# Optimization experiments

Measured on AMD Instinct MI355X. Metric: run time of the kernel, lower is better.

The kernel has to match this reference:

```python
import jax, jax.numpy as jnp
import numpy as np

B, L, V, E, H2, M, OOV = 128, 400, 50000, 512, 1024, 1024, 50


def setup_inputs() -> dict:
    key = jax.random.key(0)
    ks = jax.random.split(key, 14)
    s = 0.02
    return {
        "y": jax.random.randint(ks[0], (B,), 0, V),
        "h": jax.random.normal(ks[1], (1, B, H2), jnp.float32),
        "memory_bank": jax.random.normal(ks[2], (B, L, M), jnp.float32),
        "src_mask": jnp.ones((B, L), jnp.float32),
        "max_num_oovs": OOV,
        "src_oov": jax.random.randint(ks[3], (B, L), 0, V + OOV),
        # learned parameters (PyTorch Linear y = x @ W + b with W stored [in, out])
        "emb": jax.random.normal(ks[4], (V, E), jnp.float32) * s,
        "W_ih": jax.random.normal(ks[5], (E, 3 * H2), jnp.float32) * s,   # GRU input weights (r|z|n)
        "W_hh": jax.random.normal(ks[6], (H2, 3 * H2), jnp.float32) * s,  # GRU hidden weights (r|z|n)
        "b_ih": jnp.zeros((3 * H2,), jnp.float32),
        "b_hh": jnp.zeros((3 * H2,), jnp.float32),
        "W_mem": jax.random.normal(ks[7], (M, H2), jnp.float32) * s,      # attention memory_project (no bias)
        "W_dec": jax.random.normal(ks[8], (H2, H2), jnp.float32) * s,     # attention decode_project
        "b_dec": jnp.zeros((H2,), jnp.float32),
        "v": jax.random.normal(ks[9], (H2,), jnp.float32) * s,            # attention score vector (no bias)
        "W_pgen": jax.random.normal(ks[10], (M + H2 + E, 1), jnp.float32) * s,
        "b_pgen": jnp.zeros((1,), jnp.float32),
        "W_v1": jax.random.normal(ks[11], (M + H2, H2), jnp.float32) * s,
        "b_v1": jnp.zeros((H2,), jnp.float32),
        "W_v2": jax.random.normal(ks[12], (H2, V), jnp.float32) * s,
        "b_v2": jnp.zeros((V,), jnp.float32),
    }


def reference(y, h, memory_bank, src_mask, max_num_oovs, src_oov,
              emb, W_ih, W_hh, b_ih, b_hh, W_mem, W_dec, b_dec, v,
              W_pgen, b_pgen, W_v1, b_v1, W_v2, b_v2):
    # --- embedding lookup (single decode step) ---
    y_emb = emb[y]                                    # [B, E]
    h0 = h[-1]                                        # [B, H2]

    # --- one-step GRU (PyTorch gate order r, z, n); dropout is identity (eval) ---
    gi = y_emb @ W_ih + b_ih                          # [B, 3*H2]
    gh = h0 @ W_hh + b_hh
    i_r, i_z, i_n = jnp.split(gi, 3, axis=-1)
    h_r, h_z, h_n = jnp.split(gh, 3, axis=-1)
    r = jax.nn.sigmoid(i_r + h_r)
    z = jax.nn.sigmoid(i_z + h_z)
    n = jnp.tanh(i_n + r * h_n)
    h_next = (1.0 - z) * n + z * h0                   # [B, H2]

    # --- concat (Bahdanau) attention with masked softmax ---
    enc_feat = jnp.einsum('blm,mh->blh', memory_bank, W_mem)   # [B, L, H2]
    dec_feat = h_next @ W_dec + b_dec                           # [B, H2]
    scores = jnp.tanh(enc_feat + dec_feat[:, None, :]) @ v     # [B, L]
    attn = jax.nn.softmax(scores, axis=1) * src_mask
    attn_dist = attn / attn.sum(axis=1, keepdims=True)         # renormalized masked softmax
    context = jnp.einsum('bl,blm->bm', attn_dist, memory_bank) # [B, M]

    # --- vocab distribution ---
    vd_in = jnp.concatenate([context, h_next], axis=1)          # [B, M+H2]
    logits = (vd_in @ W_v1 + b_v1) @ W_v2 + b_v2                # [B, V]
    vocab_dist = jax.nn.softmax(logits, axis=1)

    # --- generation gate ---
    pg_in = jnp.concatenate([context, h_next, y_emb], axis=1)   # [B, M+H2+E]
    p_gen = jax.nn.sigmoid(pg_in @ W_pgen + b_pgen)             # [B, 1]

    # --- copy mechanism: scatter attention mass into extended vocab ---
    vocab_dist_ = p_gen * vocab_dist
    attn_dist_ = (1.0 - p_gen) * attn_dist
    bsz = vocab_dist_.shape[0]
    if max_num_oovs > 0:
        vocab_dist_ = jnp.concatenate(
            [vocab_dist_, jnp.zeros((bsz, max_num_oovs), vocab_dist_.dtype)], axis=1)
    rows = jnp.arange(bsz)[:, None]
    final_dist = vocab_dist_.at[rows, src_oov].add(attn_dist_)  # [B, V+OOV]

    return final_dist, h_next[None], context, attn_dist, p_gen
```

## Files before the change

### kernel.cpp

```cpp
#include <hip/hip_runtime.h>

#define B_   128
#define L_   400
#define V_   50000
#define E_   512
#define H2_  1024
#define M_   1024
#define OOV_ 50
#define VE_  50050
#define BL_  51200

typedef __attribute__((ext_vector_type(8))) short short8;
typedef __attribute__((ext_vector_type(4))) float f32x4;

__device__ __forceinline__ unsigned short f2bf(float f){
  unsigned int u = __builtin_bit_cast(unsigned int, f);
  u = (u + 0x7FFFu + ((u >> 16) & 1u)) >> 16;
  return (unsigned short)u;
}
__device__ __forceinline__ float bf2f(unsigned short s){
  unsigned int u = ((unsigned int)s) << 16;
  return __builtin_bit_cast(float, u);
}

__device__ __forceinline__ void gl_lds16(const void* g, void* l){
  __builtin_amdgcn_global_load_lds(
      (const __attribute__((address_space(1))) unsigned int*)g,
      (__attribute__((address_space(3))) unsigned int*)l, 16, 0, 0);
}

__device__ __forceinline__ float wredsum(float v){
  #pragma unroll
  for (int o = 32; o > 0; o >>= 1) v += __shfl_xor(v, o);
  return v;
}
__device__ __forceinline__ float wredmax(float v){
  #pragma unroll
  for (int o = 32; o > 0; o >>= 1) v = fmaxf(v, __shfl_xor(v, o));
  return v;
}

__global__ void embed_gather_kernel(const int* __restrict__ y, const float* __restrict__ emb,
                                    float* __restrict__ yemb){
  int idx = blockIdx.x * 256 + threadIdx.x;
  int b  = idx >> 7;
  int c4 = (idx & 127) << 2;
  float4 v = *(const float4*)(emb + (size_t)y[b] * E_ + c4);
  *(float4*)(yemb + (size_t)b * E_ + c4) = v;
}

__global__ void mb_convert_kernel(const float* __restrict__ mb, unsigned char* __restrict__ mbT){
  int u = blockIdx.x * 256 + threadIdx.x;
  int gr  = u >> 7;
  int m16 = u & 127;
  const float* src = mb + (size_t)gr * 1024 + m16 * 8;
  float4 f0 = *(const float4*)src;
  float4 f1 = *(const float4*)(src + 4);
  uint4 w;
  w.x = (unsigned)f2bf(f0.x) | ((unsigned)f2bf(f0.y) << 16);
  w.y = (unsigned)f2bf(f0.z) | ((unsigned)f2bf(f0.w) << 16);
  w.z = (unsigned)f2bf(f1.x) | ((unsigned)f2bf(f1.y) << 16);
  w.w = (unsigned)f2bf(f1.z) | ((unsigned)f2bf(f1.w) << 16);
  int panel = gr >> 7, r = gr & 127;
  int ks = m16 >> 3, c16 = m16 & 7;
  size_t dst = (size_t)panel * 262144 + (size_t)ks * 16384
             + (size_t)((r * 128 + c16 * 16) ^ ((r & 7) << 4));
  *(uint4*)(mbT + dst) = w;
}

__global__ void wmem_transposeT_kernel(const float* __restrict__ W, unsigned char* __restrict__ WTt){
  __shared__ float tile[32][33];
  int n0 = blockIdx.x * 32, k0 = blockIdx.y * 32;
  int tx = threadIdx.x, ty = threadIdx.y;
  #pragma unroll
  for (int i = 0; i < 32; i += 8) tile[ty + i][tx] = W[(size_t)(k0 + ty + i) * H2_ + n0 + tx];
  __syncthreads();
  int id = ty * 32 + tx;
  if (id < 128){
    int nn = id & 31, k16 = id >> 5;
    int col = n0 + nn, kb = k0 + k16 * 8;
    uint4 w;
    w.x = (unsigned)f2bf(tile[k16*8+0][nn]) | ((unsigned)f2bf(tile[k16*8+1][nn]) << 16);
    w.y = (unsigned)f2bf(tile[k16*8+2][nn]) | ((unsigned)f2bf(tile[k16*8+3][nn]) << 16);
    w.z = (unsigned)f2bf(tile[k16*8+4][nn]) | ((unsigned)f2bf(tile[k16*8+5][nn]) << 16);
    w.w = (unsigned)f2bf(tile[k16*8+6][nn]) | ((unsigned)f2bf(tile[k16*8+7][nn]) << 16);
    int cpn = col >> 7, r = col & 127;
    int ks = kb >> 6, c16 = (kb & 63) >> 3;
    size_t dst = (size_t)cpn * 262144 + (size_t)ks * 16384
               + (size_t)((r * 128 + c16 * 16) ^ ((r & 7) << 4));
    *(uint4*)(WTt + dst) = w;
  }
}

__launch_bounds__(256)
__global__ void gemm128_kernel(const float* __restrict__ A, int lda,
                               const float* __restrict__ W, int ldw,
                               const float* __restrict__ bias,
                               float* __restrict__ C, int ldc,
                               int N, int kChunk, int addBias)
{
  int tid = threadIdx.x;
  int wv = tid >> 6, lane = tid & 63, lr = lane & 15, lhi = lane >> 4;
  int colBase = blockIdx.x * 128 + wv * 32;
  int colL[2];
  colL[0] = min(colBase + lr, N - 1);
  colL[1] = min(colBase + 16 + lr, N - 1);
  int k0 = blockIdx.y * kChunk;

  f32x4 zero = {0.f, 0.f, 0.f, 0.f};
  f32x4 acc[8][2];
  #pragma unroll
  for (int r = 0; r < 8; r++){ acc[r][0] = zero; acc[r][1] = zero; }

  int nks = kChunk >> 5;
  for (int ks = 0; ks < nks; ++ks){
    int k = k0 + ks * 32 + lhi * 8;
    short8 bf[2];
    #pragma unroll
    for (int cf = 0; cf < 2; cf++){
      #pragma unroll
      for (int j = 0; j < 8; j++)
        bf[cf][j] = (short)f2bf(W[(size_t)(k + j) * ldw + colL[cf]]);
    }
    #pragma unroll
    for (int rf = 0; rf < 8; rf++){
      const float* ap = A + (size_t)(rf * 16 + lr) * lda + k;
      float4 a0 = *(const float4*)ap;
      float4 a1 = *(const float4*)(ap + 4);
      short8 af;
      af[0]=(short)f2bf(a0.x); af[1]=(short)f2bf(a0.y); af[2]=(short)f2bf(a0.z); af[3]=(short)f2bf(a0.w);
      af[4]=(short)f2bf(a1.x); af[5]=(short)f2bf(a1.y); af[6]=(short)f2bf(a1.z); af[7]=(short)f2bf(a1.w);
      acc[rf][0] = __builtin_amdgcn_mfma_f32_16x16x32_bf16(af, bf[0], acc[rf][0], 0, 0, 0);
      acc[rf][1] = __builtin_amdgcn_mfma_f32_16x16x32_bf16(af, bf[1], acc[rf][1], 0, 0, 0);
    }
  }

  bool addB = addBias && (blockIdx.y == 0);
  #pragma unroll
  for (int cf = 0; cf < 2; cf++){
    int col = colBase + cf * 16 + lr;
    bool ok = col < N;
    float bv = addB ? bias[colL[cf]] : 0.f;
    #pragma unroll
    for (int rf = 0; rf < 8; rf++)
      #pragma unroll
      for (int i = 0; i < 4; i++){
        int row = rf * 16 + lhi * 4 + i;
        if (ok) atomicAdd(&C[(size_t)row * ldc + col], acc[rf][cf][i] + bv);
      }
  }
}

__launch_bounds__(256)
__global__ void gemm_v1_kernel(const float* __restrict__ A1, const float* __restrict__ A2,
                               const float* __restrict__ W,
                               const float* __restrict__ bias,
                               float* __restrict__ C, int N, int kChunk)
{
  int tid = threadIdx.x;
  int wv = tid >> 6, lane = tid & 63, lr = lane & 15, lhi = lane >> 4;
  int colBase = blockIdx.x * 128 + wv * 32;
  int halfY = gridDim.y >> 1;
  const float* Asrc = (blockIdx.y < halfY) ? A1 : A2;
  int yk = (blockIdx.y < halfY) ? blockIdx.y : (blockIdx.y - halfY);
  int k0 = yk * kChunk;
  int wk0 = blockIdx.y * kChunk;

  f32x4 zero = {0.f, 0.f, 0.f, 0.f};
  f32x4 acc[8][2];
  #pragma unroll
  for (int r = 0; r < 8; r++){ acc[r][0] = zero; acc[r][1] = zero; }

  int nks = kChunk >> 5;
  for (int ks = 0; ks < nks; ++ks){
    int k  = k0 + ks * 32 + lhi * 8;
    int wk = wk0 + ks * 32 + lhi * 8;
    short8 bf[2];
    #pragma unroll
    for (int cf = 0; cf < 2; cf++){
      #pragma unroll
      for (int j = 0; j < 8; j++)
        bf[cf][j] = (short)f2bf(W[(size_t)(wk + j) * H2_ + colBase + cf * 16 + lr]);
    }
    #pragma unroll
    for (int rf = 0; rf < 8; rf++){
      const float* ap = Asrc + (size_t)(rf * 16 + lr) * 1024 + k;
      float4 a0 = *(const float4*)ap;
      float4 a1 = *(const float4*)(ap + 4);
      short8 af;
      af[0]=(short)f2bf(a0.x); af[1]=(short)f2bf(a0.y); af[2]=(short)f2bf(a0.z); af[3]=(short)f2bf(a0.w);
      af[4]=(short)f2bf(a1.x); af[5]=(short)f2bf(a1.y); af[6]=(short)f2bf(a1.z); af[7]=(short)f2bf(a1.w);
      acc[rf][0] = __builtin_amdgcn_mfma_f32_16x16x32_bf16(af, bf[0], acc[rf][0], 0, 0, 0);
      acc[rf][1] = __builtin_amdgcn_mfma_f32_16x16x32_bf16(af, bf[1], acc[rf][1], 0, 0, 0);
    }
  }

  bool addB = (blockIdx.y == 0);
  #pragma unroll
  for (int cf = 0; cf < 2; cf++){
    int col = colBase + cf * 16 + lr;
    float bv = addB ? bias[col] : 0.f;
    #pragma unroll
    for (int rf = 0; rf < 8; rf++)
      #pragma unroll
      for (int i = 0; i < 4; i++){
        int row = rf * 16 + lhi * 4 + i;
        atomicAdd(&C[(size_t)row * H2_ + col], acc[rf][cf][i] + bv);
      }
  }
}

__launch_bounds__(256)
__global__ void gemm_bfA_kernel(const unsigned short* __restrict__ A,
                                const float* __restrict__ W,
                                const float* __restrict__ bias,
                                float* __restrict__ C0, float* __restrict__ C1,
                                int N, int kChunk)
{
  int tid = threadIdx.x;
  int wv = tid >> 6, lane = tid & 63, lr = lane & 15, lhi = lane >> 4;
  int colBase = blockIdx.x * 128 + wv * 32;
  int colL[2];
  colL[0] = min(colBase + lr, N - 1);
  colL[1] = min(colBase + 16 + lr, N - 1);
  int k0 = blockIdx.y * kChunk;
  float* Cw = (blockIdx.y == 0) ? C0 : C1;

  f32x4 zero = {0.f, 0.f, 0.f, 0.f};
  f32x4 acc[8][2];
  #pragma unroll
  for (int r = 0; r < 8; r++){ acc[r][0] = zero; acc[r][1] = zero; }

  int nks = kChunk >> 5;
  for (int ks = 0; ks < nks; ++ks){
    int k = k0 + ks * 32 + lhi * 8;
    short8 bf[2];
    #pragma unroll
    for (int cf = 0; cf < 2; cf++){
      #pragma unroll
      for (int j = 0; j < 8; j++)
        bf[cf][j] = (short)f2bf(W[(size_t)(k + j) * N + colL[cf]]);
    }
    #pragma unroll
    for (int rf = 0; rf < 8; rf++){
      short8 af = *(const short8*)(A + (size_t)(rf * 16 + lr) * 1024 + k);
      acc[rf][0] = __builtin_amdgcn_mfma_f32_16x16x32_bf16(af, bf[0], acc[rf][0], 0, 0, 0);
      acc[rf][1] = __builtin_amdgcn_mfma_f32_16x16x32_bf16(af, bf[1], acc[rf][1], 0, 0, 0);
    }
  }

  bool addB = (blockIdx.y == 0);
  #pragma unroll
  for (int cf = 0; cf < 2; cf++){
    int col = colBase + cf * 16 + lr;
    bool ok = col < N;
    float bv = addB ? bias[colL[cf]] : 0.f;
    #pragma unroll
    for (int rf = 0; rf < 8; rf++)
      #pragma unroll
      for (int i = 0; i < 4; i++){
        int row = rf * 16 + lhi * 4 + i;
        if (ok) Cw[(size_t)row * V_ + col] = acc[rf][cf][i] + bv;
      }
  }
}

__global__ void gru_gates_kernel(const float* __restrict__ gi, const float* __restrict__ gh,
                                 const float* __restrict__ bih, const float* __restrict__ bhh,
                                 const float* __restrict__ h0, float* __restrict__ hn){
  int idx = blockIdx.x * 256 + threadIdx.x;
  int b = idx >> 10, j = idx & 1023;
  const float* gib = gi + (size_t)b * 3072;
  const float* ghb = gh + (size_t)b * 3072;
  float ir = gib[j]        + bih[j],        hr = ghb[j]        + bhh[j];
  float iz = gib[j + 1024] + bih[j + 1024], hz = ghb[j + 1024] + bhh[j + 1024];
  float in_= gib[j + 2048] + bih[j + 2048], hnv= ghb[j + 2048] + bhh[j + 2048];
  float r = 1.f / (1.f + __expf(-(ir + hr)));
  float z = 1.f / (1.f + __expf(-(iz + hz)));
  float n = tanhf(in_ + r * hnv);
  hn[idx] = (1.f - z) * n + z * h0[idx];
}

__launch_bounds__(512, 3)
__global__ void scores_kernel(const unsigned char* __restrict__ mbT,
                              const unsigned char* __restrict__ WTt,
                              const float* __restrict__ dec, const float* __restrict__ vvec,
                              float* __restrict__ scr)
{
  __shared__ __align__(16) unsigned char LDSm[65536];
  const int tid = threadIdx.x, lane = tid & 63;
  const int wv = tid >> 6, lr = lane & 15, lhi = lane >> 4;
  const int wru = wv >> 2, wcu = wv & 3;

  int p = blockIdx.x;
  int lid = (p & 7) * 400 + (p >> 3);
  int rp = lid >> 3, cp = lid & 7;
  int r0 = rp << 7;

  int wvu = __builtin_amdgcn_readfirstlane(wv);
  const unsigned char* seg = (wvu < 4 ? mbT + (size_t)rp * 262144
                                      : WTt + (size_t)cp * 262144)
                             + (wvu & 3) * 4096 + lane * 16;
  const int segLds = (wvu & 3) * 4096 + (wvu < 4 ? 0 : 16384);

  int aoff[4], boff[2];
  #pragma unroll
  for (int rf = 0; rf < 4; rf++){
    int row = wru * 64 + rf * 16 + lr;
    aoff[rf] = (row * 128 + lhi * 16) ^ ((row & 7) << 4);
  }
  #pragma unroll
  for (int cf = 0; cf < 2; cf++){
    int col = wcu * 32 + cf * 16 + lr;
    boff[cf] = ((col * 128 + lhi * 16) ^ ((col & 7) << 4)) + 16384;
  }

  f32x4 zero = {0.f, 0.f, 0.f, 0.f};
  f32x4 acc[4][2];
  #pragma unroll
  for (int rf = 0; rf < 4; rf++){ acc[rf][0] = zero; acc[rf][1] = zero; }

  #pragma unroll
  for (int j = 0; j < 4; j++)
    gl_lds16(seg + j * 1024, &LDSm[segLds + j * 1024]);

  #pragma unroll 1
  for (int t = 0; t < 16; ++t){
    const int cur = (t & 1) << 15;
    if (t < 15){
      const unsigned char* s = seg + (size_t)(t + 1) * 16384;
      const int nb = ((t + 1) & 1) << 15;
      #pragma unroll
      for (int j = 0; j < 4; j++)
        gl_lds16(s + j * 1024, &LDSm[nb + segLds + j * 1024]);
      asm volatile("s_waitcnt vmcnt(4)" ::: "memory");
    } else {
      asm volatile("s_waitcnt vmcnt(0)" ::: "memory");
    }
    __builtin_amdgcn_sched_barrier(0);
    __builtin_amdgcn_s_barrier();
    __builtin_amdgcn_sched_barrier(0);
    #pragma unroll
    for (int k2 = 0; k2 < 2; k2++){
      short8 af[4], bfr[2];
      #pragma unroll
      for (int rf = 0; rf < 4; rf++) af[rf]  = *(const short8*)&LDSm[cur + (aoff[rf] ^ (k2 << 6))];
      #pragma unroll
      for (int cf = 0; cf < 2; cf++) bfr[cf] = *(const short8*)&LDSm[cur + (boff[cf] ^ (k2 << 6))];
      __builtin_amdgcn_s_setprio(1);
      #pragma unroll
      for (int rf = 0; rf < 4; rf++)
        #pragma unroll
        for (int cf = 0; cf < 2; cf++)
          acc[rf][cf] = __builtin_amdgcn_mfma_f32_16x16x32_bf16(af[rf], bfr[cf], acc[rf][cf], 0, 0, 0);
      __builtin_amdgcn_s_setprio(0);
    }
    __builtin_amdgcn_sched_barrier(0);
    asm volatile("s_waitcnt lgkmcnt(0)" ::: "memory");
    __builtin_amdgcn_s_barrier();
    __builtin_amdgcn_sched_barrier(0);
  }

  int colb = (cp << 7) + wcu * 32 + lr;
  float vv0 = vvec[colb], vv1 = vvec[colb + 16];
  #pragma unroll
  for (int rf = 0; rf < 4; rf++){
    #pragma unroll
    for (int i = 0; i < 4; i++){
      int grow = r0 + wru * 64 + rf * 16 + lhi * 4 + i;
      int bb = grow / 400;
      const float* dp = dec + (size_t)bb * 1024 + colb;
      float x0 = acc[rf][0][i] + dp[0];
      float x1 = acc[rf][1][i] + dp[16];
      float part = (1.f - 2.f / (__expf(2.f * x0) + 1.f)) * vv0
                 + (1.f - 2.f / (__expf(2.f * x1) + 1.f)) * vv1;
      part += __shfl_xor(part, 1);
      part += __shfl_xor(part, 2);
      part += __shfl_xor(part, 4);
      part += __shfl_xor(part, 8);
      if (lr == 0) atomicAdd(&scr[grow], part);
    }
  }
}

__global__ void attn_softmax_kernel(const float* __restrict__ scores, const float* __restrict__ mask,
                                    float* __restrict__ attn){
  int b = blockIdx.x, t = threadIdx.x;
  int wv = t >> 6, lane = t & 63;
  __shared__ float red[4];
  float s0 = (t < 400)       ? scores[b * 400 + t]       : -1e30f;
  float s1 = (t + 256 < 400) ? scores[b * 400 + t + 256] : -1e30f;
  float m = wredmax(fmaxf(s0, s1));
  if (lane == 0) red[wv] = m;
  __syncthreads();
  float M = fmaxf(fmaxf(red[0], red[1]), fmaxf(red[2], red[3]));
  __syncthreads();
  float e0 = (t < 400)       ? __expf(s0 - M) * mask[b * 400 + t]       : 0.f;
  float e1 = (t + 256 < 400) ? __expf(s1 - M) * mask[b * 400 + t + 256] : 0.f;
  float s = wredsum(e0 + e1);
  if (lane == 0) red[wv] = s;
  __syncthreads();
  float inv = 1.f / (red[0] + red[1] + red[2] + red[3]);
  if (t < 400)       attn[b * 400 + t]       = e0 * inv;
  if (t + 256 < 400) attn[b * 400 + t + 256] = e1 * inv;
}

__launch_bounds__(256)
__global__ void context_kernel(const float* __restrict__ attn, const unsigned char* __restrict__ mbT,
                               float* __restrict__ ctx){
  int b = blockIdx.y, lc = blockIdx.x, t = threadIdx.x;
  int u = t & 127;
  int half = t >> 7;
  __shared__ float a[100];
  if (t < 100) a[t] = attn[b * 400 + lc * 100 + t];
  __syncthreads();
  int ks = u >> 3, c16 = u & 7;
  float s[8];
  #pragma unroll
  for (int j = 0; j < 8; j++) s[j] = 0.f;
  for (int l = half; l < 100; l += 2){
    int gr = b * 400 + lc * 100 + l;
    int panel = gr >> 7, r = gr & 127;
    const unsigned char* pp = mbT + (size_t)panel * 262144 + (size_t)ks * 16384
                              + (size_t)((r * 128 + c16 * 16) ^ ((r & 7) << 4));
    short8 v = *(const short8*)pp;
    float al = a[l];
    #pragma unroll
    for (int j = 0; j < 8; j++) s[j] += al * bf2f((unsigned short)v[j]);
  }
  float* cp = ctx + (size_t)b * M_ + u * 8;
  #pragma unroll
  for (int j = 0; j < 8; j++) atomicAdd(cp + j, s[j]);
}

__global__ void pgen_kernel(const float* __restrict__ ctx, const float* __restrict__ hn,
                            const float* __restrict__ yemb,
                            const float* __restrict__ Wp, const float* __restrict__ bp,
                            float* __restrict__ pg){
  int b = blockIdx.x, t = threadIdx.x, wv = t >> 6, lane = t & 63;
  __shared__ float red[4];
  float s = 0.f;
  for (int i = t; i < 1024; i += 256) s += ctx[(size_t)b * 1024 + i] * Wp[i];
  for (int i = t; i < 1024; i += 256) s += hn[(size_t)b * 1024 + i] * Wp[1024 + i];
  for (int i = t; i < 512;  i += 256) s += yemb[(size_t)b * 512 + i] * Wp[2048 + i];
  s = wredsum(s);
  if (lane == 0) red[wv] = s;
  __syncthreads();
  if (t == 0){
    float S = red[0] + red[1] + red[2] + red[3] + bp[0];
    pg[b] = 1.f / (1.f + __expf(-S));
  }
}

__global__ void hid2bf_kernel(const float* __restrict__ hid, unsigned short* __restrict__ hb){
  int idx = blockIdx.x * 256 + threadIdx.x;
  float4 v = *(const float4*)(hid + (size_t)idx * 4);
  ushort2 p0 = {f2bf(v.x), f2bf(v.y)};
  ushort2 p1 = {f2bf(v.z), f2bf(v.w)};
  *(ushort2*)(hb + (size_t)idx * 4)     = p0;
  *(ushort2*)(hb + (size_t)idx * 4 + 2) = p1;
}

__global__ void vocab_softmax_kernel(float* __restrict__ lg0, const float* __restrict__ lg1,
                                     const float* __restrict__ pg,
                                     const float* __restrict__ attn, const int* __restrict__ soov,
                                     float* __restrict__ fin){
  int b = blockIdx.x, t = threadIdx.x, wv = t >> 6, lane = t & 63;
  __shared__ float redm[16], reds[16];
  float* l0 = lg0 + (size_t)b * V_;
  const float* l1 = lg1 + (size_t)b * V_;
  float m = -1e30f, s = 0.f;
  for (int i = t; i < V_; i += 1024){
    float l = l0[i] + l1[i];
    l0[i] = l;
    float mn = fmaxf(m, l);
    s = s * __expf(m - mn) + __expf(l - mn);
    m = mn;
  }
  #pragma unroll
  for (int o = 32; o > 0; o >>= 1){
    float mo = __shfl_xor(m, o), so = __shfl_xor(s, o);
    float mn = fmaxf(m, mo);
    s = s * __expf(m - mn) + so * __expf(mo - mn);
    m = mn;
  }
  if (lane == 0){ redm[wv] = m; reds[wv] = s; }
  __syncthreads();
  float M = -1e30f;
  #pragma unroll
  for (int w = 0; w < 16; w++) M = fmaxf(M, redm[w]);
  float S = 0.f;
  #pragma unroll
  for (int w = 0; w < 16; w++) S += reds[w] * __expf(redm[w] - M);
  float pgb = pg[b];
  float scale = pgb / S;
  float* fb = fin + (size_t)b * VE_;
  for (int i = t; i < V_; i += 1024) fb[i] = __expf(l0[i] - M) * scale;
  for (int i = V_ + t; i < VE_; i += 1024) fb[i] = 0.f;
  __syncthreads();
  float om = 1.f - pgb;
  if (t < 400) atomicAdd(&fb[soov[b * 400 + t]], om * attn[b * 400 + t]);
}

extern "C" void kernel_launch(void* const* d_in, const int* in_sizes, int n_in,
                              void* d_out, int out_size, void* d_ws, size_t ws_size,
                              hipStream_t stream)
{
  const int*   y     = (const int*)  d_in[0];
  const float* hin   = (const float*)d_in[1];
  const float* mb    = (const float*)d_in[2];
  const float* mask  = (const float*)d_in[3];
  const int*   soov  = (const int*)  d_in[5];
  const float* emb   = (const float*)d_in[6];
  const float* W_ih  = (const float*)d_in[7];
  const float* W_hh  = (const float*)d_in[8];
  const float* b_ih  = (const float*)d_in[9];
  const float* b_hh  = (const float*)d_in[10];
  const float* W_mem = (const float*)d_in[11];
  const float* W_dec = (const float*)d_in[12];
  const float* b_dec = (const float*)d_in[13];
  const float* vvec  = (const float*)d_in[14];
  const float* W_pg  = (const float*)d_in[15];
  const float* b_pg  = (const float*)d_in[16];
  const float* W_v1  = (const float*)d_in[17];
  const float* b_v1  = (const float*)d_in[18];
  const float* W_v2  = (const float*)d_in[19];
  const float* b_v2  = (const float*)d_in[20];

  float* out   = (float*)d_out;
  float* fin   = out;
  float* hnext = out + (size_t)B_ * VE_;
  float* ctx   = hnext + (size_t)B_ * H2_;
  float* attn  = ctx + (size_t)B_ * M_;
  float* pg    = attn + (size_t)B_ * L_;

  float* ws   = (float*)d_ws;
  float* yemb = ws;
  float* gi   = ws + 65536;
  float* gh   = gi + 393216;
  float* dec  = gh + 393216;
  float* scr  = dec + 131072;
  float* hid  = scr + 51200;
  float* lg0  = hid + 131072;
  unsigned short* hidbf = (unsigned short*)(lg0 + 6400000);
  unsigned char*  WTt   = (unsigned char*)(hidbf + 131072);
  unsigned char*  mbT   = WTt + 2097152;
  float* lg1  = (float*)mbT;

  hipMemsetAsync(gi, 0, (size_t)(393216 + 393216 + 131072 + 51200) * 4, stream);
  hipMemsetAsync(hid, 0, (size_t)131072 * 4, stream);
  hipMemsetAsync(ctx, 0, (size_t)B_ * M_ * 4, stream);

  embed_gather_kernel<<<64, 256, 0, stream>>>(y, emb, yemb);
  wmem_transposeT_kernel<<<dim3(32, 32), dim3(32, 8), 0, stream>>>(W_mem, WTt);
  mb_convert_kernel<<<25600, 256, 0, stream>>>(mb, mbT);

  gemm128_kernel<<<dim3(24, 2), 256, 0, stream>>>(yemb, E_,  W_ih, 3 * H2_, nullptr, gi, 3 * H2_, 3 * H2_, 256, 0);
  gemm128_kernel<<<dim3(24, 4), 256, 0, stream>>>(hin,  H2_, W_hh, 3 * H2_, nullptr, gh, 3 * H2_, 3 * H2_, 256, 0);
  gru_gates_kernel<<<512, 256, 0, stream>>>(gi, gh, b_ih, b_hh, hin, hnext);
  gemm128_kernel<<<dim3(8, 4), 256, 0, stream>>>(hnext, H2_, W_dec, H2_, b_dec, dec, H2_, H2_, 256, 1);

  scores_kernel<<<3200, 512, 0, stream>>>(mbT, WTt, dec, vvec, scr);
  attn_softmax_kernel<<<128, 256, 0, stream>>>(scr, mask, attn);
  context_kernel<<<dim3(4, 128), 256, 0, stream>>>(attn, mbT, ctx);

  pgen_kernel<<<128, 256, 0, stream>>>(ctx, hnext, yemb, W_pg, b_pg, pg);
  gemm_v1_kernel<<<dim3(8, 8), 256, 0, stream>>>(ctx, hnext, W_v1, b_v1, hid, H2_, 256);
  hid2bf_kernel<<<128, 256, 0, stream>>>(hid, hidbf);
  gemm_bfA_kernel<<<dim3(391, 2), 256, 0, stream>>>(hidbf, W_v2, b_v2, lg0, lg1, V_, 512);

  vocab_softmax_kernel<<<128, 1024, 0, stream>>>(lg0, lg1, pg, attn, soov, fin);
}
```

Baseline: 598.0 us.

## Fuse small launches and overlap memory-bank conversion with GRU GEMMs

Merges the memset, embedding gather, W_mem transpose and part of the memory-bank bf16 conversion into one pre-kernel. The rest of the conversion is split into chunks that ride along with the GRU GEMM, gate and decode-projection kernels, so the bandwidth-bound conversion overlaps the small, under-occupied GEMMs. The attention softmax is folded into the context kernel, and p_gen is folded into the W_v1 GEMM kernel, which now writes per-K-slice partials instead of using atomics. This cuts launch count and idle time, at the cost of heterogeneous blocks inside each kernel and more complex buffer aliasing.

```diff
diff --git a/kernel.cpp b/kernel.cpp
--- a/kernel.cpp
+++ b/kernel.cpp
@@ -40,17 +40,8 @@
   return v;
 }
 
-__global__ void embed_gather_kernel(const int* __restrict__ y, const float* __restrict__ emb,
-                                    float* __restrict__ yemb){
-  int idx = blockIdx.x * 256 + threadIdx.x;
-  int b  = idx >> 7;
-  int c4 = (idx & 127) << 2;
-  float4 v = *(const float4*)(emb + (size_t)y[b] * E_ + c4);
-  *(float4*)(yemb + (size_t)b * E_ + c4) = v;
-}
-
-__global__ void mb_convert_kernel(const float* __restrict__ mb, unsigned char* __restrict__ mbT){
-  int u = blockIdx.x * 256 + threadIdx.x;
+__device__ __forceinline__ void mb_convert_unit(const float* __restrict__ mb,
+                                                unsigned char* __restrict__ mbT, int u){
   int gr  = u >> 7;
   int m16 = u & 127;
   const float* src = mb + (size_t)gr * 1024 + m16 * 8;
@@ -68,32 +59,56 @@
   *(uint4*)(mbT + dst) = w;
 }
 
-__global__ void wmem_transposeT_kernel(const float* __restrict__ W, unsigned char* __restrict__ WTt){
+__global__ void pre_kernel(const float* __restrict__ mb, unsigned char* __restrict__ mbT,
+                           const float* __restrict__ Wm, unsigned char* __restrict__ WTt,
+                           const int* __restrict__ y, const float* __restrict__ emb,
+                           float* __restrict__ yemb, float* __restrict__ zeroA,
+                           float* __restrict__ ctx)
+{
   __shared__ float tile[32][33];
-  int n0 = blockIdx.x * 32, k0 = blockIdx.y * 32;
-  int tx = threadIdx.x, ty = threadIdx.y;
-  #pragma unroll
-  for (int i = 0; i < 32; i += 8) tile[ty + i][tx] = W[(size_t)(k0 + ty + i) * H2_ + n0 + tx];
-  __syncthreads();
-  int id = ty * 32 + tx;
-  if (id < 128){
-    int nn = id & 31, k16 = id >> 5;
-    int col = n0 + nn, kb = k0 + k16 * 8;
-    uint4 w;
-    w.x = (unsigned)f2bf(tile[k16*8+0][nn]) | ((unsigned)f2bf(tile[k16*8+1][nn]) << 16);
-    w.y = (unsigned)f2bf(tile[k16*8+2][nn]) | ((unsigned)f2bf(tile[k16*8+3][nn]) << 16);
-    w.z = (unsigned)f2bf(tile[k16*8+4][nn]) | ((unsigned)f2bf(tile[k16*8+5][nn]) << 16);
-    w.w = (unsigned)f2bf(tile[k16*8+6][nn]) | ((unsigned)f2bf(tile[k16*8+7][nn]) << 16);
-    int cpn = col >> 7, r = col & 127;
-    int ks = kb >> 6, c16 = (kb & 63) >> 3;
-    size_t dst = (size_t)cpn * 262144 + (size_t)ks * 16384
-               + (size_t)((r * 128 + c16 * 16) ^ ((r & 7) << 4));
-    *(uint4*)(WTt + dst) = w;
-  }
-}
-
-__launch_bounds__(256)
-__global__ void gemm128_kernel(const float* __restrict__ A, int lda,
+  int bid = blockIdx.x, t = threadIdx.x;
+  if (bid < 6400){
+    mb_convert_unit(mb, mbT, bid * 256 + t);
+  } else if (bid < 7424){
+    int b2 = bid - 6400;
+    int n0 = (b2 & 31) * 32, k0 = (b2 >> 5) * 32;
+    int tx = t & 31, ty = t >> 5;
+    #pragma unroll
+    for (int i = 0; i < 32; i += 8) tile[ty + i][tx] = Wm[(size_t)(k0 + ty + i) * H2_ + n0 + tx];
+    __syncthreads();
+    if (t < 128){
+      int nn = t & 31, k16 = t >> 5;
+      int col = n0 + nn, kb = k0 + k16 * 8;
+      uint4 w;
+      w.x = (unsigned)f2bf(tile[k16*8+0][nn]) | ((unsigned)f2bf(tile[k16*8+1][nn]) << 16);
+      w.y = (unsigned)f2bf(tile[k16*8+2][nn]) | ((unsigned)f2bf(tile[k16*8+3][nn]) << 16);
+      w.z = (unsigned)f2bf(tile[k16*8+4][nn]) | ((unsigned)f2bf(tile[k16*8+5][nn]) << 16);
+      w.w = (unsigned)f2bf(tile[k16*8+6][nn]) | ((unsigned)f2bf(tile[k16*8+7][nn]) << 16);
+      int cpn = col >> 7, r = col & 127;
+      int ks = kb >> 6, c16 = (kb & 63) >> 3;
+      size_t dst = (size_t)cpn * 262144 + (size_t)ks * 16384
+                 + (size_t)((r * 128 + c16 * 16) ^ ((r & 7) << 4));
+      *(uint4*)(WTt + dst) = w;
+    }
+  } else if (bid < 7488){
+    int idx = (bid - 7424) * 256 + t;
+    int b  = idx >> 7;
+    int c4 = (idx & 127) << 2;
+    float4 v = *(const float4*)(emb + (size_t)y[b] * E_ + c4);
+    *(float4*)(yemb + (size_t)b * E_ + c4) = v;
+  } else if (bid < 8434){
+    int u = (bid - 7488) * 256 + t;
+    float4 z = {0.f, 0.f, 0.f, 0.f};
+    *(float4*)(zeroA + (size_t)u * 4) = z;
+  } else {
+    int u = (bid - 8434) * 256 + t;
+    float4 z = {0.f, 0.f, 0.f, 0.f};
+    *(float4*)(ctx + (size_t)u * 4) = z;
+  }
+}
+
+__device__ __forceinline__ void gemm128_body(int bx, int by,
+                               const float* __restrict__ A, int lda,
                                const float* __restrict__ W, int ldw,
                                const float* __restrict__ bias,
                                float* __restrict__ C, int ldc,
@@ -101,11 +116,11 @@
 {
   int tid = threadIdx.x;
   int wv = tid >> 6, lane = tid & 63, lr = lane & 15, lhi = lane >> 4;
-  int colBase = blockIdx.x * 128 + wv * 32;
+  int colBase = bx * 128 + wv * 32;
   int colL[2];
   colL[0] = min(colBase + lr, N - 1);
   colL[1] = min(colBase + 16 + lr, N - 1);
-  int k0 = blockIdx.y * kChunk;
+  int k0 = by * kChunk;
 
   f32x4 zero = {0.f, 0.f, 0.f, 0.f};
   f32x4 acc[8][2];
@@ -135,7 +150,7 @@
     }
   }
 
-  bool addB = addBias && (blockIdx.y == 0);
+  bool addB = addBias && (by == 0);
   #pragma unroll
   for (int cf = 0; cf < 2; cf++){
     int col = colBase + cf * 16 + lr;
@@ -152,62 +167,292 @@
 }
 
 __launch_bounds__(256)
-__global__ void gemm_v1_kernel(const float* __restrict__ A1, const float* __restrict__ A2,
-                               const float* __restrict__ W,
-                               const float* __restrict__ bias,
-                               float* __restrict__ C, int N, int kChunk)
+__global__ void gigh_kernel(const float* __restrict__ yemb, const float* __restrict__ hin,
+                            const float* __restrict__ W_ih, const float* __restrict__ W_hh,
+                            float* __restrict__ gi, float* __restrict__ gh,
+                            const float* __restrict__ mb, unsigned char* __restrict__ mbT){
+  int bid = blockIdx.x;
+  if (bid < 48)
+    gemm128_body(bid % 24, bid / 24, yemb, E_,  W_ih, 3 * H2_, nullptr, gi, 3 * H2_, 3 * H2_, 256, 0);
+  else if (bid < 144){
+    int b2 = bid - 48;
+    gemm128_body(b2 % 24, b2 / 24, hin, H2_, W_hh, 3 * H2_, nullptr, gh, 3 * H2_, 3 * H2_, 256, 0);
+  } else {
+    mb_convert_unit(mb, mbT, (6400 + bid - 144) * 256 + threadIdx.x);
+  }
+}
+
+__global__ void gru_gates_kernel(const float* __restrict__ gi, const float* __restrict__ gh,
+                                 const float* __restrict__ bih, const float* __restrict__ bhh,
+                                 const float* __restrict__ h0, float* __restrict__ hn,
+                                 const float* __restrict__ mb, unsigned char* __restrict__ mbT){
+  int bid = blockIdx.x;
+  if (bid >= 512){
+    mb_convert_unit(mb, mbT, (12800 + bid - 512) * 256 + threadIdx.x);
+    return;
+  }
+  int idx = bid * 256 + threadIdx.x;
+  int b = idx >> 10, j = idx & 1023;
+  const float* gib = gi + (size_t)b * 3072;
+  const float* ghb = gh + (size_t)b * 3072;
+  float ir = gib[j]        + bih[j],        hr = ghb[j]        + bhh[j];
+  float iz = gib[j + 1024] + bih[j + 1024], hz = ghb[j + 1024] + bhh[j + 1024];
+  float in_= gib[j + 2048] + bih[j + 2048], hnv= ghb[j + 2048] + bhh[j + 2048];
+  float r = 1.f / (1.f + __expf(-(ir + hr)));
+  float z = 1.f / (1.f + __expf(-(iz + hz)));
+  float n = tanhf(in_ + r * hnv);
+  hn[idx] = (1.f - z) * n + z * h0[idx];
+}
+
+__launch_bounds__(256)
+__global__ void dec_kernel(const float* __restrict__ hnext, const float* __restrict__ W_dec,
+                           const float* __restrict__ b_dec, float* __restrict__ dec,
+                           const float* __restrict__ mb, unsigned char* __restrict__ mbT){
+  int bid = blockIdx.x;
+  if (bid < 32)
+    gemm128_body(bid & 7, bid >> 3, hnext, H2_, W_dec, H2_, b_dec, dec, H2_, H2_, 256, 1);
+  else
+    mb_convert_unit(mb, mbT, (19200 + bid - 32) * 256 + threadIdx.x);
+}
+
+__launch_bounds__(512, 3)
+__global__ void scores_kernel(const unsigned char* __restrict__ mbT,
+                              const unsigned char* __restrict__ WTt,
+                              const float* __restrict__ dec, const float* __restrict__ vvec,
+                              float* __restrict__ scr)
 {
-  int tid = threadIdx.x;
-  int wv = tid >> 6, lane = tid & 63, lr = lane & 15, lhi = lane >> 4;
-  int colBase = blockIdx.x * 128 + wv * 32;
-  int halfY = gridDim.y >> 1;
-  const float* Asrc = (blockIdx.y < halfY) ? A1 : A2;
-  int yk = (blockIdx.y < halfY) ? blockIdx.y : (blockIdx.y - halfY);
-  int k0 = yk * kChunk;
-  int wk0 = blockIdx.y * kChunk;
+  __shared__ __align__(16) unsigned char LDSm[65536];
+  const int tid = threadIdx.x, lane = tid & 63;
+  const int wv = tid >> 6, lr = lane & 15, lhi = lane >> 4;
+  const int wru = wv >> 2, wcu = wv & 3;
+
+  int p = blockIdx.x;
+  int lid = (p & 7) * 400 + (p >> 3);
+  int rp = lid >> 3, cp = lid & 7;
+  int r0 = rp << 7;
+
+  int wvu = __builtin_amdgcn_readfirstlane(wv);
+  const unsigned char* seg = (wvu < 4 ? mbT + (size_t)rp * 262144
+                                      : WTt + (size_t)cp * 262144)
+                             + (wvu & 3) * 4096 + lane * 16;
+  const int segLds = (wvu & 3) * 4096 + (wvu < 4 ? 0 : 16384);
+
+  int aoff[4], boff[2];
+  #pragma unroll
+  for (int rf = 0; rf < 4; rf++){
+    int row = wru * 64 + rf * 16 + lr;
+    aoff[rf] = (row * 128 + lhi * 16) ^ ((row & 7) << 4);
+  }
+  #pragma unroll
+  for (int cf = 0; cf < 2; cf++){
+    int col = wcu * 32 + cf * 16 + lr;
+    boff[cf] = ((col * 128 + lhi * 16) ^ ((col & 7) << 4)) + 16384;
+  }
 
   f32x4 zero = {0.f, 0.f, 0.f, 0.f};
-  f32x4 acc[8][2];
-  #pragma unroll
-  for (int r = 0; r < 8; r++){ acc[r][0] = zero; acc[r][1] = zero; }
-
-  int nks = kChunk >> 5;
-  for (int ks = 0; ks < nks; ++ks){
-    int k  = k0 + ks * 32 + lhi * 8;
-    int wk = wk0 + ks * 32 + lhi * 8;
-    short8 bf[2];
+  f32x4 acc[4][2];
+  #pragma unroll
+  for (int rf = 0; rf < 4; rf++){ acc[rf][0] = zero; acc[rf][1] = zero; }
+
+  #pragma unroll
+  for (int j = 0; j < 4; j++)
+    gl_lds16(seg + j * 1024, &LDSm[segLds + j * 1024]);
+
+  #pragma unroll 1
+  for (int t = 0; t < 16; ++t){
+    const int cur = (t & 1) << 15;
+    if (t < 15){
+      const unsigned char* s = seg + (size_t)(t + 1) * 16384;
+      const int nb = ((t + 1) & 1) << 15;
+      #pragma unroll
+      for (int j = 0; j < 4; j++)
+        gl_lds16(s + j * 1024, &LDSm[nb + segLds + j * 1024]);
+      asm volatile("s_waitcnt vmcnt(4)" ::: "memory");
+    } else {
+      asm volatile("s_waitcnt vmcnt(0)" ::: "memory");
+    }
+    __builtin_amdgcn_sched_barrier(0);
+    __builtin_amdgcn_s_barrier();
+    __builtin_amdgcn_sched_barrier(0);
+    #pragma unroll
+    for (int k2 = 0; k2 < 2; k2++){
+      short8 af[4], bfr[2];
+      #pragma unroll
+      for (int rf = 0; rf < 4; rf++) af[rf]  = *(const short8*)&LDSm[cur + (aoff[rf] ^ (k2 << 6))];
+      #pragma unroll
+      for (int cf = 0; cf < 2; cf++) bfr[cf] = *(const short8*)&LDSm[cur + (boff[cf] ^ (k2 << 6))];
+      __builtin_amdgcn_s_setprio(1);
+      #pragma unroll
+      for (int rf = 0; rf < 4; rf++)
+        #pragma unroll
+        for (int cf = 0; cf < 2; cf++)
+          acc[rf][cf] = __builtin_amdgcn_mfma_f32_16x16x32_bf16(af[rf], bfr[cf], acc[rf][cf], 0, 0, 0);
+      __builtin_amdgcn_s_setprio(0);
+    }
+    __builtin_amdgcn_sched_barrier(0);
+    asm volatile("s_waitcnt lgkmcnt(0)" ::: "memory");
+    __builtin_amdgcn_s_barrier();
+    __builtin_amdgcn_sched_barrier(0);
+  }
+
+  int colb = (cp << 7) + wcu * 32 + lr;
+  float vv0 = vvec[colb], vv1 = vvec[colb + 16];
+  #pragma unroll
+  for (int rf = 0; rf < 4; rf++){
+    #pragma unroll
+    for (int i = 0; i < 4; i++){
+      int grow = r0 + wru * 64 + rf * 16 + lhi * 4 + i;
+      int bb = grow / 400;
+      const float* dp = dec + (size_t)bb * 1024 + colb;
+      float x0 = acc[rf][0][i] + dp[0];
+      float x1 = acc[rf][1][i] + dp[16];
+      float part = (1.f - 2.f / (__expf(2.f * x0) + 1.f)) * vv0
+                 + (1.f - 2.f / (__expf(2.f * x1) + 1.f)) * vv1;
+      part += __shfl_xor(part, 1);
+      part += __shfl_xor(part, 2);
+      part += __shfl_xor(part, 4);
+      part += __shfl_xor(part, 8);
+      if (lr == 0) atomicAdd(&scr[grow], part);
+    }
+  }
+}
+
+__launch_bounds__(256)
+__global__ void context_kernel(const float* __restrict__ scr, const float* __restrict__ mask,
+                               const unsigned char* __restrict__ mbT,
+                               float* __restrict__ ctx, float* __restrict__ attn){
+  int b = blockIdx.y, lc = blockIdx.x, t = threadIdx.x;
+  int wv = t >> 6, lane = t & 63;
+  __shared__ float red[4];
+  __shared__ float a[400];
+  float s0 = scr[b * 400 + t];
+  float s1 = (t < 144) ? scr[b * 400 + t + 256] : -1e30f;
+  float m = wredmax(fmaxf(s0, s1));
+  if (lane == 0) red[wv] = m;
+  __syncthreads();
+  float M = fmaxf(fmaxf(red[0], red[1]), fmaxf(red[2], red[3]));
+  __syncthreads();
+  float e0 = __expf(s0 - M) * mask[b * 400 + t];
+  float e1 = (t < 144) ? __expf(s1 - M) * mask[b * 400 + t + 256] : 0.f;
+  float s = wredsum(e0 + e1);
+  if (lane == 0) red[wv] = s;
+  __syncthreads();
+  float inv = 1.f / (red[0] + red[1] + red[2] + red[3]);
+  a[t] = e0 * inv;
+  if (t < 144) a[t + 256] = e1 * inv;
+  __syncthreads();
+  if (t < 100) attn[b * 400 + lc * 100 + t] = a[lc * 100 + t];
+
+  int u = t & 127;
+  int half = t >> 7;
+  int ks = u >> 3, c16 = u & 7;
+  float sa[8];
+  #pragma unroll
+  for (int j = 0; j < 8; j++) sa[j] = 0.f;
+  for (int l = half; l < 100; l += 2){
+    int gr = b * 400 + lc * 100 + l;
+    int panel = gr >> 7, r = gr & 127;
+    const unsigned char* pp = mbT + (size_t)panel * 262144 + (size_t)ks * 16384
+                              + (size_t)((r * 128 + c16 * 16) ^ ((r & 7) << 4));
+    short8 v = *(const short8*)pp;
+    float al = a[lc * 100 + l];
+    #pragma unroll
+    for (int j = 0; j < 8; j++) sa[j] += al * bf2f((unsigned short)v[j]);
+  }
+  float* cp = ctx + (size_t)b * M_ + u * 8;
+  #pragma unroll
+  for (int j = 0; j < 8; j++) atomicAdd(cp + j, sa[j]);
+}
+
+__launch_bounds__(256)
+__global__ void v1_pgen_kernel(const float* __restrict__ ctx, const float* __restrict__ hn,
+                               const float* __restrict__ yemb,
+                               const float* __restrict__ Wv1, const float* __restrict__ bv1,
+                               float* __restrict__ vp,
+                               const float* __restrict__ Wp, const float* __restrict__ bp,
+                               float* __restrict__ pg)
+{
+  int bid = blockIdx.x;
+  if (bid < 64){
+    int bx = bid & 7, by = bid >> 3;
+    int tid = threadIdx.x;
+    int wv = tid >> 6, lane = tid & 63, lr = lane & 15, lhi = lane >> 4;
+    int colBase = bx * 128 + wv * 32;
+    const float* Asrc = (by < 4) ? ctx : hn;
+    int k0 = ((by < 4) ? by : (by - 4)) * 256;
+    int wk0 = by * 256;
+
+    f32x4 zero = {0.f, 0.f, 0.f, 0.f};
+    f32x4 acc[8][2];
+    #pragma unroll
+    for (int r = 0; r < 8; r++){ acc[r][0] = zero; acc[r][1] = zero; }
+
+    for (int ks = 0; ks < 8; ++ks){
+      int k  = k0 + ks * 32 + lhi * 8;
+      int wk = wk0 + ks * 32 + lhi * 8;
+      short8 bf[2];
+      #pragma unroll
+      for (int cf = 0; cf < 2; cf++){
+        #pragma unroll
+        for (int j = 0; j < 8; j++)
+          bf[cf][j] = (short)f2bf(Wv1[(size_t)(wk + j) * H2_ + colBase + cf * 16 + lr]);
+      }
+      #pragma unroll
+      for (int rf = 0; rf < 8; rf++){
+        const float* ap = Asrc + (size_t)(rf * 16 + lr) * 1024 + k;
+        float4 a0 = *(const float4*)ap;
+        float4 a1 = *(const float4*)(ap + 4);
+        short8 af;
+        af[0]=(short)f2bf(a0.x); af[1]=(short)f2bf(a0.y); af[2]=(short)f2bf(a0.z); af[3]=(short)f2bf(a0.w);
+        af[4]=(short)f2bf(a1.x); af[5]=(short)f2bf(a1.y); af[6]=(short)f2bf(a1.z); af[7]=(short)f2bf(a1.w);
+        acc[rf][0] = __builtin_amdgcn_mfma_f32_16x16x32_bf16(af, bf[0], acc[rf][0], 0, 0, 0);
+        acc[rf][1] = __builtin_amdgcn_mfma_f32_16x16x32_bf16(af, bf[1], acc[rf][1], 0, 0, 0);
+      }
+    }
+
+    float* Cw = vp + (size_t)by * 131072;
+    bool addB = (by == 0);
     #pragma unroll
     for (int cf = 0; cf < 2; cf++){
-      #pragma unroll
-      for (int j = 0; j < 8; j++)
-        bf[cf][j] = (short)f2bf(W[(size_t)(wk + j) * H2_ + colBase + cf * 16 + lr]);
-    }
-    #pragma unroll
-    for (int rf = 0; rf < 8; rf++){
-      const float* ap = Asrc + (size_t)(rf * 16 + lr) * 1024 + k;
-      float4 a0 = *(const float4*)ap;
-      float4 a1 = *(const float4*)(ap + 4);
-      short8 af;
-      af[0]=(short)f2bf(a0.x); af[1]=(short)f2bf(a0.y); af[2]=(short)f2bf(a0.z); af[3]=(short)f2bf(a0.w);
-      af[4]=(short)f2bf(a1.x); af[5]=(short)f2bf(a1.y); af[6]=(short)f2bf(a1.z); af[7]=(short)f2bf(a1.w);
-      acc[rf][0] = __builtin_amdgcn_mfma_f32_16x16x32_bf16(af, bf[0], acc[rf][0], 0, 0, 0);
-      acc[rf][1] = __builtin_amdgcn_mfma_f32_16x16x32_bf16(af, bf[1], acc[rf][1], 0, 0, 0);
-    }
-  }
-
-  bool addB = (blockIdx.y == 0);
-  #pragma unroll
-  for (int cf = 0; cf < 2; cf++){
-    int col = colBase + cf * 16 + lr;
-    float bv = addB ? bias[col] : 0.f;
-    #pragma unroll
-    for (int rf = 0; rf < 8; rf++)
-      #pragma unroll
-      for (int i = 0; i < 4; i++){
-        int row = rf * 16 + lhi * 4 + i;
-        atomicAdd(&C[(size_t)row * H2_ + col], acc[rf][cf][i] + bv);
-      }
-  }
+      int col = colBase + cf * 16 + lr;
+      float bv = addB ? bv1[col] : 0.f;
+      #pragma unroll
+      for (int rf = 0; rf < 8; rf++)
+        #pragma unroll
+        for (int i = 0; i < 4; i++){
+          int row = rf * 16 + lhi * 4 + i;
+          Cw[(size_t)row * H2_ + col] = acc[rf][cf][i] + bv;
+        }
+    }
+  } else {
+    int b = bid - 64, t = threadIdx.x, wv = t >> 6, lane = t & 63;
+    __shared__ float red[4];
+    float s = 0.f;
+    for (int i = t; i < 1024; i += 256) s += ctx[(size_t)b * 1024 + i] * Wp[i];
+    for (int i = t; i < 1024; i += 256) s += hn[(size_t)b * 1024 + i] * Wp[1024 + i];
+    for (int i = t; i < 512;  i += 256) s += yemb[(size_t)b * 512 + i] * Wp[2048 + i];
+    s = wredsum(s);
+    if (lane == 0) red[wv] = s;
+    __syncthreads();
+    if (t == 0){
+      float S = red[0] + red[1] + red[2] + red[3] + bp[0];
+      pg[b] = 1.f / (1.f + __expf(-S));
+    }
+  }
+}
+
+__global__ void hid2bf_kernel(const float* __restrict__ vp, unsigned short* __restrict__ hb){
+  int id = blockIdx.x * 256 + threadIdx.x;
+  float4 s = *(const float4*)(vp + (size_t)id * 4);
+  #pragma unroll
+  for (int ky = 1; ky < 8; ky++){
+    float4 v = *(const float4*)(vp + (size_t)ky * 131072 + (size_t)id * 4);
+    s.x += v.x; s.y += v.y; s.z += v.z; s.w += v.w;
+  }
+  ushort2 p0 = {f2bf(s.x), f2bf(s.y)};
+  ushort2 p1 = {f2bf(s.z), f2bf(s.w)};
+  *(ushort2*)(hb + (size_t)id * 4)     = p0;
+  *(ushort2*)(hb + (size_t)id * 4 + 2) = p1;
 }
 
 __launch_bounds__(256)
@@ -263,202 +508,6 @@
         if (ok) Cw[(size_t)row * V_ + col] = acc[rf][cf][i] + bv;
       }
   }
-}
-
-__global__ void gru_gates_kernel(const float* __restrict__ gi, const float* __restrict__ gh,
-                                 const float* __restrict__ bih, const float* __restrict__ bhh,
-                                 const float* __restrict__ h0, float* __restrict__ hn){
-  int idx = blockIdx.x * 256 + threadIdx.x;
-  int b = idx >> 10, j = idx & 1023;
-  const float* gib = gi + (size_t)b * 3072;
-  const float* ghb = gh + (size_t)b * 3072;
-  float ir = gib[j]        + bih[j],        hr = ghb[j]        + bhh[j];
-  float iz = gib[j + 1024] + bih[j + 1024], hz = ghb[j + 1024] + bhh[j + 1024];
-  float in_= gib[j + 2048] + bih[j + 2048], hnv= ghb[j + 2048] + bhh[j + 2048];
-  float r = 1.f / (1.f + __expf(-(ir + hr)));
-  float z = 1.f / (1.f + __expf(-(iz + hz)));
-  float n = tanhf(in_ + r * hnv);
-  hn[idx] = (1.f - z) * n + z * h0[idx];
-}
-
-__launch_bounds__(512, 3)
-__global__ void scores_kernel(const unsigned char* __restrict__ mbT,
-                              const unsigned char* __restrict__ WTt,
-                              const float* __restrict__ dec, const float* __restrict__ vvec,
-                              float* __restrict__ scr)
-{
-  __shared__ __align__(16) unsigned char LDSm[65536];
-  const int tid = threadIdx.x, lane = tid & 63;
-  const int wv = tid >> 6, lr = lane & 15, lhi = lane >> 4;
-  const int wru = wv >> 2, wcu = wv & 3;
-
-  int p = blockIdx.x;
-  int lid = (p & 7) * 400 + (p >> 3);
-  int rp = lid >> 3, cp = lid & 7;
-  int r0 = rp << 7;
-
-  int wvu = __builtin_amdgcn_readfirstlane(wv);
-  const unsigned char* seg = (wvu < 4 ? mbT + (size_t)rp * 262144
-                                      : WTt + (size_t)cp * 262144)
-                             + (wvu & 3) * 4096 + lane * 16;
-  const int segLds = (wvu & 3) * 4096 + (wvu < 4 ? 0 : 16384);
-
-  int aoff[4], boff[2];
-  #pragma unroll
-  for (int rf = 0; rf < 4; rf++){
-    int row = wru * 64 + rf * 16 + lr;
-    aoff[rf] = (row * 128 + lhi * 16) ^ ((row & 7) << 4);
-  }
-  #pragma unroll
-  for (int cf = 0; cf < 2; cf++){
-    int col = wcu * 32 + cf * 16 + lr;
-    boff[cf] = ((col * 128 + lhi * 16) ^ ((col & 7) << 4)) + 16384;
-  }
-
-  f32x4 zero = {0.f, 0.f, 0.f, 0.f};
-  f32x4 acc[4][2];
-  #pragma unroll
-  for (int rf = 0; rf < 4; rf++){ acc[rf][0] = zero; acc[rf][1] = zero; }
-
-  #pragma unroll
-  for (int j = 0; j < 4; j++)
-    gl_lds16(seg + j * 1024, &LDSm[segLds + j * 1024]);
-
-  #pragma unroll 1
-  for (int t = 0; t < 16; ++t){
-    const int cur = (t & 1) << 15;
-    if (t < 15){
-      const unsigned char* s = seg + (size_t)(t + 1) * 16384;
-      const int nb = ((t + 1) & 1) << 15;
-      #pragma unroll
-      for (int j = 0; j < 4; j++)
-        gl_lds16(s + j * 1024, &LDSm[nb + segLds + j * 1024]);
-      asm volatile("s_waitcnt vmcnt(4)" ::: "memory");
-    } else {
-      asm volatile("s_waitcnt vmcnt(0)" ::: "memory");
-    }
-    __builtin_amdgcn_sched_barrier(0);
-    __builtin_amdgcn_s_barrier();
-    __builtin_amdgcn_sched_barrier(0);
-    #pragma unroll
-    for (int k2 = 0; k2 < 2; k2++){
-      short8 af[4], bfr[2];
-      #pragma unroll
-      for (int rf = 0; rf < 4; rf++) af[rf]  = *(const short8*)&LDSm[cur + (aoff[rf] ^ (k2 << 6))];
-      #pragma unroll
-      for (int cf = 0; cf < 2; cf++) bfr[cf] = *(const short8*)&LDSm[cur + (boff[cf] ^ (k2 << 6))];
-      __builtin_amdgcn_s_setprio(1);
-      #pragma unroll
-      for (int rf = 0; rf < 4; rf++)
-        #pragma unroll
-        for (int cf = 0; cf < 2; cf++)
-          acc[rf][cf] = __builtin_amdgcn_mfma_f32_16x16x32_bf16(af[rf], bfr[cf], acc[rf][cf], 0, 0, 0);
-      __builtin_amdgcn_s_setprio(0);
-    }
-    __builtin_amdgcn_sched_barrier(0);
-    asm volatile("s_waitcnt lgkmcnt(0)" ::: "memory");
-    __builtin_amdgcn_s_barrier();
-    __builtin_amdgcn_sched_barrier(0);
-  }
-
-  int colb = (cp << 7) + wcu * 32 + lr;
-  float vv0 = vvec[colb], vv1 = vvec[colb + 16];
-  #pragma unroll
-  for (int rf = 0; rf < 4; rf++){
-    #pragma unroll
-    for (int i = 0; i < 4; i++){
-      int grow = r0 + wru * 64 + rf * 16 + lhi * 4 + i;
-      int bb = grow / 400;
-      const float* dp = dec + (size_t)bb * 1024 + colb;
-      float x0 = acc[rf][0][i] + dp[0];
-      float x1 = acc[rf][1][i] + dp[16];
-      float part = (1.f - 2.f / (__expf(2.f * x0) + 1.f)) * vv0
-                 + (1.f - 2.f / (__expf(2.f * x1) + 1.f)) * vv1;
-      part += __shfl_xor(part, 1);
-      part += __shfl_xor(part, 2);
-      part += __shfl_xor(part, 4);
-      part += __shfl_xor(part, 8);
-      if (lr == 0) atomicAdd(&scr[grow], part);
-    }
-  }
-}
-
-__global__ void attn_softmax_kernel(const float* __restrict__ scores, const float* __restrict__ mask,
-                                    float* __restrict__ attn){
-  int b = blockIdx.x, t = threadIdx.x;
-  int wv = t >> 6, lane = t & 63;
-  __shared__ float red[4];
-  float s0 = (t < 400)       ? scores[b * 400 + t]       : -1e30f;
-  float s1 = (t + 256 < 400) ? scores[b * 400 + t + 256] : -1e30f;
-  float m = wredmax(fmaxf(s0, s1));
-  if (lane == 0) red[wv] = m;
-  __syncthreads();
-  float M = fmaxf(fmaxf(red[0], red[1]), fmaxf(red[2], red[3]));
-  __syncthreads();
-  float e0 = (t < 400)       ? __expf(s0 - M) * mask[b * 400 + t]       : 0.f;
-  float e1 = (t + 256 < 400) ? __expf(s1 - M) * mask[b * 400 + t + 256] : 0.f;
-  float s = wredsum(e0 + e1);
-  if (lane == 0) red[wv] = s;
-  __syncthreads();
-  float inv = 1.f / (red[0] + red[1] + red[2] + red[3]);
-  if (t < 400)       attn[b * 400 + t]       = e0 * inv;
-  if (t + 256 < 400) attn[b * 400 + t + 256] = e1 * inv;
-}
-
-__launch_bounds__(256)
-__global__ void context_kernel(const float* __restrict__ attn, const unsigned char* __restrict__ mbT,
-                               float* __restrict__ ctx){
-  int b = blockIdx.y, lc = blockIdx.x, t = threadIdx.x;
-  int u = t & 127;
-  int half = t >> 7;
-  __shared__ float a[100];
-  if (t < 100) a[t] = attn[b * 400 + lc * 100 + t];
-  __syncthreads();
-  int ks = u >> 3, c16 = u & 7;
-  float s[8];
-  #pragma unroll
-  for (int j = 0; j < 8; j++) s[j] = 0.f;
-  for (int l = half; l < 100; l += 2){
-    int gr = b * 400 + lc * 100 + l;
-    int panel = gr >> 7, r = gr & 127;
-    const unsigned char* pp = mbT + (size_t)panel * 262144 + (size_t)ks * 16384
-                              + (size_t)((r * 128 + c16 * 16) ^ ((r & 7) << 4));
-    short8 v = *(const short8*)pp;
-    float al = a[l];
-    #pragma unroll
-    for (int j = 0; j < 8; j++) s[j] += al * bf2f((unsigned short)v[j]);
-  }
-  float* cp = ctx + (size_t)b * M_ + u * 8;
-  #pragma unroll
-  for (int j = 0; j < 8; j++) atomicAdd(cp + j, s[j]);
-}
-
-__global__ void pgen_kernel(const float* __restrict__ ctx, const float* __restrict__ hn,
-                            const float* __restrict__ yemb,
-                            const float* __restrict__ Wp, const float* __restrict__ bp,
-                            float* __restrict__ pg){
-  int b = blockIdx.x, t = threadIdx.x, wv = t >> 6, lane = t & 63;
-  __shared__ float red[4];
-  float s = 0.f;
-  for (int i = t; i < 1024; i += 256) s += ctx[(size_t)b * 1024 + i] * Wp[i];
-  for (int i = t; i < 1024; i += 256) s += hn[(size_t)b * 1024 + i] * Wp[1024 + i];
-  for (int i = t; i < 512;  i += 256) s += yemb[(size_t)b * 512 + i] * Wp[2048 + i];
-  s = wredsum(s);
-  if (lane == 0) red[wv] = s;
-  __syncthreads();
-  if (t == 0){
-    float S = red[0] + red[1] + red[2] + red[3] + bp[0];
-    pg[b] = 1.f / (1.f + __expf(-S));
-  }
-}
-
-__global__ void hid2bf_kernel(const float* __restrict__ hid, unsigned short* __restrict__ hb){
-  int idx = blockIdx.x * 256 + threadIdx.x;
-  float4 v = *(const float4*)(hid + (size_t)idx * 4);
-  ushort2 p0 = {f2bf(v.x), f2bf(v.y)};
-  ushort2 p1 = {f2bf(v.z), f2bf(v.w)};
-  *(ushort2*)(hb + (size_t)idx * 4)     = p0;
-  *(ushort2*)(hb + (size_t)idx * 4 + 2) = p1;
 }
 
 __global__ void vocab_softmax_kernel(float* __restrict__ lg0, const float* __restrict__ lg1,
@@ -540,33 +589,23 @@
   float* gh   = gi + 393216;
   float* dec  = gh + 393216;
   float* scr  = dec + 131072;
-  float* hid  = scr + 51200;
-  float* lg0  = hid + 131072;
+  float* lg0  = scr + 51200;
+  float* vp   = lg0;
   unsigned short* hidbf = (unsigned short*)(lg0 + 6400000);
   unsigned char*  WTt   = (unsigned char*)(hidbf + 131072);
   unsigned char*  mbT   = WTt + 2097152;
   float* lg1  = (float*)mbT;
 
-  hipMemsetAsync(gi, 0, (size_t)(393216 + 393216 + 131072 + 51200) * 4, stream);
-  hipMemsetAsync(hid, 0, (size_t)131072 * 4, stream);
-  hipMemsetAsync(ctx, 0, (size_t)B_ * M_ * 4, stream);
-
-  embed_gather_kernel<<<64, 256, 0, stream>>>(y, emb, yemb);
-  wmem_transposeT_kernel<<<dim3(32, 32), dim3(32, 8), 0, stream>>>(W_mem, WTt);
-  mb_convert_kernel<<<25600, 256, 0, stream>>>(mb, mbT);
-
-  gemm128_kernel<<<dim3(24, 2), 256, 0, stream>>>(yemb, E_,  W_ih, 3 * H2_, nullptr, gi, 3 * H2_, 3 * H2_, 256, 0);
-  gemm128_kernel<<<dim3(24, 4), 256, 0, stream>>>(hin,  H2_, W_hh, 3 * H2_, nullptr, gh, 3 * H2_, 3 * H2_, 256, 0);
-  gru_gates_kernel<<<512, 256, 0, stream>>>(gi, gh, b_ih, b_hh, hin, hnext);
-  gemm128_kernel<<<dim3(8, 4), 256, 0, stream>>>(hnext, H2_, W_dec, H2_, b_dec, dec, H2_, H2_, 256, 1);
+  pre_kernel<<<8562, 256, 0, stream>>>(mb, mbT, W_mem, WTt, y, emb, yemb, gi, ctx);
+  gigh_kernel<<<6544, 256, 0, stream>>>(yemb, hin, W_ih, W_hh, gi, gh, mb, mbT);
+  gru_gates_kernel<<<6912, 256, 0, stream>>>(gi, gh, b_ih, b_hh, hin, hnext, mb, mbT);
+  dec_kernel<<<6432, 256, 0, stream>>>(hnext, W_dec, b_dec, dec, mb, mbT);
 
   scores_kernel<<<3200, 512, 0, stream>>>(mbT, WTt, dec, vvec, scr);
-  attn_softmax_kernel<<<128, 256, 0, stream>>>(scr, mask, attn);
-  context_kernel<<<dim3(4, 128), 256, 0, stream>>>(attn, mbT, ctx);
-
-  pgen_kernel<<<128, 256, 0, stream>>>(ctx, hnext, yemb, W_pg, b_pg, pg);
-  gemm_v1_kernel<<<dim3(8, 8), 256, 0, stream>>>(ctx, hnext, W_v1, b_v1, hid, H2_, 256);
-  hid2bf_kernel<<<128, 256, 0, stream>>>(hid, hidbf);
+  context_kernel<<<dim3(4, 128), 256, 0, stream>>>(scr, mask, mbT, ctx, attn);
+
+  v1_pgen_kernel<<<192, 256, 0, stream>>>(ctx, hnext, yemb, W_v1, b_v1, vp, W_pg, b_pg, pg);
+  hid2bf_kernel<<<128, 256, 0, stream>>>(vp, hidbf);
   gemm_bfA_kernel<<<dim3(391, 2), 256, 0, stream>>>(hidbf, W_v2, b_v2, lg0, lg1, V_, 512);
 
   vocab_softmax_kernel<<<128, 1024, 0, stream>>>(lg0, lg1, pg, attn, soov, fin);
```

New measurement: 521.0 us. 1.15x faster.
